# Optimization experiments

Measured on AMD Instinct MI355X. Metric: run time of the kernel, lower is better.

The kernel has to match this reference:

```python
import jax, jax.numpy as jnp
import numpy as np

B, S, DIM, HEADS, EXPERTS = 2, 2048, 1024, 16, 8
DFF = 4 * DIM
EPS = 1e-5


def setup_inputs() -> dict:
    key = jax.random.key(0)
    ks = jax.random.split(key, 16)
    w = lambda k, shp: jax.random.normal(k, shp, dtype=jnp.float32) * 0.02
    return {
        "x": jax.random.normal(ks[0], (B, S, DIM), dtype=jnp.float32),
        "ln1_g": jnp.ones((DIM,), jnp.float32), "ln1_b": jnp.zeros((DIM,), jnp.float32),
        "ln2_g": jnp.ones((DIM,), jnp.float32), "ln2_b": jnp.zeros((DIM,), jnp.float32),
        "wq": w(ks[1], (DIM, DIM)), "bq": jnp.zeros((DIM,), jnp.float32),
        "wk": w(ks[2], (DIM, DIM)), "bk": jnp.zeros((DIM,), jnp.float32),
        "wv": w(ks[3], (DIM, DIM)), "bv": jnp.zeros((DIM,), jnp.float32),
        "wo": w(ks[4], (DIM, DIM)), "bo": jnp.zeros((DIM,), jnp.float32),
        "w1": w(ks[5], (EXPERTS, DIM, DFF)), "b1": jnp.zeros((EXPERTS, DFF), jnp.float32),
        "w2": w(ks[6], (EXPERTS, DFF, DIM)), "b2": jnp.zeros((EXPERTS, DIM), jnp.float32),
        "token_split": np.full(EXPERTS, S // EXPERTS, dtype=np.int64),  # static split sizes
        "heads": HEADS,
    }


def _layernorm(h, g, b):
    m = h.mean(-1, keepdims=True)
    v = ((h - m) ** 2).mean(-1, keepdims=True)
    return (h - m) * jax.lax.rsqrt(v + EPS) * g + b


def reference(x, ln1_g, ln1_b, ln2_g, ln2_b, wq, bq, wk, bk, wv, bv, wo, bo,
              w1, b1, w2, b2, token_split, heads):
    Bx, Sx, D = x.shape
    Dh = D // heads
    # --- attention on norm1(x) ---
    h = _layernorm(x, ln1_g, ln1_b)
    q = (h @ wq + bq).reshape(Bx, Sx, heads, Dh)
    k = (h @ wk + bk).reshape(Bx, Sx, heads, Dh)
    v = (h @ wv + bv).reshape(Bx, Sx, heads, Dh)
    scores = jnp.einsum('bqhd,bkhd->bhqk', q, k) * (Dh ** -0.5)
    attn = jax.nn.softmax(scores, axis=-1)
    o = jnp.einsum('bhqk,bkhd->bqhd', attn, v).reshape(Bx, Sx, D)
    x = x + (o @ wo + bo)
    # --- token-chunked per-expert MLP ---
    residual = x
    h = _layernorm(x, ln2_g, ln2_b)
    split_pts = np.cumsum(np.asarray(token_split))[:-1]  # static boundaries
    chunks = jnp.split(h, split_pts, axis=1)
    outs = [jax.nn.silu(c @ w1[e] + b1[e]) @ w2[e] + b2[e]
            for e, c in enumerate(chunks)]
    return jnp.concatenate(outs, axis=1) + residual
```

## Files before the change

### kernel.cpp

```cpp
#include <hip/hip_runtime.h>


typedef unsigned int  u32;
typedef unsigned short u16;
typedef short v8s __attribute__((ext_vector_type(8)));
typedef float v4f __attribute__((ext_vector_type(4)));

#define SEQ  2048
#define DIM_ 1024
#define EPS_ 1e-5f

__device__ __forceinline__ u16 f2bf(float f) {
    __bf16 h = (__bf16)f;
    return __builtin_bit_cast(u16, h);
}

__device__ __forceinline__ void gload16(const void* g, void* l) {
    __builtin_amdgcn_global_load_lds((const __attribute__((address_space(1))) u32*)g,
                                     (__attribute__((address_space(3))) u32*)l, 16, 0, 0);
}

__global__ __launch_bounds__(256) void ln_kernel(const float* __restrict__ x,
                                                 const float* __restrict__ g,
                                                 const float* __restrict__ b,
                                                 u16* __restrict__ out) {
    int row = blockIdx.x;
    int t = threadIdx.x;
    const float4* xr = (const float4*)(x + (size_t)row * DIM_);
    float4 v = xr[t];
    float s  = v.x + v.y + v.z + v.w;
    float ss = v.x*v.x + v.y*v.y + v.z*v.z + v.w*v.w;
    #pragma unroll
    for (int off = 32; off > 0; off >>= 1) {
        s  += __shfl_down(s, off);
        ss += __shfl_down(ss, off);
    }
    __shared__ float red[8];
    if ((t & 63) == 0) { red[t >> 6] = s; red[4 + (t >> 6)] = ss; }
    __syncthreads();
    s  = red[0] + red[1] + red[2] + red[3];
    ss = red[4] + red[5] + red[6] + red[7];
    float mean = s * (1.0f / DIM_);
    float var  = ss * (1.0f / DIM_) - mean * mean;
    float rstd = rsqrtf(var + EPS_);
    float4 gv = ((const float4*)g)[t];
    float4 bv = ((const float4*)b)[t];
    ushort4 ov;
    ov.x = f2bf((v.x - mean) * rstd * gv.x + bv.x);
    ov.y = f2bf((v.y - mean) * rstd * gv.y + bv.y);
    ov.z = f2bf((v.z - mean) * rstd * gv.z + bv.z);
    ov.w = f2bf((v.w - mean) * rstd * gv.w + bv.w);
    *(ushort4*)(out + (size_t)row * DIM_ + t * 4) = ov;
}

template<int BN, int ACT, bool GROUPED, int WMODE>
__global__ __launch_bounds__(256) void gemm_bf16(
    const u16* __restrict__ A,
    const float* __restrict__ W0, const float* __restrict__ Wk, const float* __restrict__ Wv,
    const float* __restrict__ b0, const float* __restrict__ bk2, const float* __restrict__ bv2,
    const float* __restrict__ resid, float* __restrict__ Cf,
    u16* __restrict__ Cb, u16* __restrict__ Ckb, u16* __restrict__ vtb,
    int Nw, int K)
{
    constexpr int BM = 128;
    constexpr int MI = 4;
    constexpr int NI = BN / 32;
    constexpr int SL = BN / 32;
    __shared__ __attribute__((aligned(16))) char AsB[BM * 128];
    __shared__ __attribute__((aligned(16))) char BsB[BN * 128];

    int tid = threadIdx.x;
    int lane = tid & 63, w = tid >> 6;
    int wr = w >> 1, wc = w & 1;
    int g = lane >> 4, lq = lane & 15;

    long row0; const float* W = W0; const float* bias = b0;
    if (GROUPED) {
        int seg = blockIdx.y >> 1, mh = blockIdx.y & 1;
        int bb = seg >> 3, e = seg & 7;
        row0 = (long)bb * SEQ + e * 256 + mh * BM;
        W += (size_t)e * K * Nw; bias += (size_t)e * Nw;
    } else row0 = (long)blockIdx.y * BM;

    int col0 = blockIdx.x * BN;
    int colL = col0;
    if (WMODE == 2) {
        int sel = col0 >> 10; colL = col0 & 1023;
        if (sel == 1)      { W = Wk; bias = bk2; }
        else if (sel == 2) { W = Wv; bias = bv2; }
    }

    const u16* Arow = A + row0 * K;

    v4f acc[MI][NI];
    #pragma unroll
    for (int mi = 0; mi < MI; mi++)
        #pragma unroll
        for (int ni = 0; ni < NI; ni++) acc[mi][ni] = (v4f){0.f, 0.f, 0.f, 0.f};

    int nB = tid & (BN - 1);
    int sgB = tid / BN;

    for (int kt = 0; kt < K; kt += 64) {
        #pragma unroll
        for (int i = 0; i < 4; i++) {
            int row  = (i * 4 + w) * 8 + (lane >> 3);
            int scol = ((lane & 7) ^ (row & 7)) << 3;
            gload16(Arow + (size_t)row * K + kt + scol, AsB + (i * 4 + w) * 1024);
        }
        #pragma unroll
        for (int i = 0; i < SL; i++) {
            int s = sgB * SL + i;
            float fv[8];
            #pragma unroll
            for (int j = 0; j < 8; j++)
                fv[j] = W[(size_t)(kt + s * 8 + j) * Nw + colL + nB];
            union { v8s v; u16 u[8]; } pk;
            #pragma unroll
            for (int j = 0; j < 8; j++) pk.u[j] = f2bf(fv[j]);
            *(v8s*)(BsB + nB * 128 + ((s ^ (nB & 7)) << 4)) = pk.v;
        }
        __syncthreads();
        #pragma unroll
        for (int kk = 0; kk < 64; kk += 32) {
            v8s af[MI], bfv[NI];
            int slot = (kk >> 3) + g;
            #pragma unroll
            for (int mi = 0; mi < MI; mi++) {
                int row = wr * 64 + mi * 16 + lq;
                af[mi] = *(const v8s*)(AsB + row * 128 + ((slot ^ (row & 7)) << 4));
            }
            #pragma unroll
            for (int ni = 0; ni < NI; ni++) {
                int rn = wc * (BN / 2) + ni * 16 + lq;
                bfv[ni] = *(const v8s*)(BsB + rn * 128 + ((slot ^ (rn & 7)) << 4));
            }
            #pragma unroll
            for (int mi = 0; mi < MI; mi++)
                #pragma unroll
                for (int ni = 0; ni < NI; ni++)
                    acc[mi][ni] = __builtin_amdgcn_mfma_f32_16x16x32_bf16(
                        af[mi], bfv[ni], acc[mi][ni], 0, 0, 0);
        }
        __syncthreads();
    }

    #pragma unroll
    for (int mi = 0; mi < MI; mi++) {
        int grow = wr * 64 + mi * 16 + g * 4;
        #pragma unroll
        for (int ni = 0; ni < NI; ni++) {
            int cL = colL + wc * (BN / 2) + ni * 16 + lq;
            float bb_ = bias[cL];
            v4f a = acc[mi][ni];
            if (WMODE == 0) {
                #pragma unroll
                for (int r = 0; r < 4; r++) {
                    float val = a[r] + bb_;
                    if (ACT == 1) val = val / (1.0f + __expf(-val));
                    size_t idx = (size_t)(row0 + grow + r) * Nw + cL;
                    val += resid[idx];
                    Cf[idx] = val;
                }
            } else if (WMODE == 1) {
                #pragma unroll
                for (int r = 0; r < 4; r++) {
                    float val = a[r] + bb_;
                    if (ACT == 1) val = val / (1.0f + __expf(-val));
                    Cb[(size_t)(row0 + grow + r) * Nw + cL] = f2bf(val);
                }
            } else {
                int sel = col0 >> 10;
                if (sel < 2) {
                    u16* dst = (sel == 0) ? Cb : Ckb;
                    #pragma unroll
                    for (int r = 0; r < 4; r++)
                        dst[(size_t)(row0 + grow + r) * 1024 + cL] = f2bf(a[r] + bb_);
                } else {
                    long token0 = row0 + grow;
                    int bb2 = (int)(token0 >> 11);
                    int ss  = (int)(token0 & 2047);
                    int hh = cL >> 6, dd = cL & 63;
                    ushort4 pv_;
                    pv_.x = f2bf(a[0] + bb_); pv_.y = f2bf(a[1] + bb_);
                    pv_.z = f2bf(a[2] + bb_); pv_.w = f2bf(a[3] + bb_);
                    *(ushort4*)(vtb + ((size_t)(bb2 * 16 + hh) * 64 + dd) * 2048 + ss) = pv_;
                }
            }
        }
    }
}

__global__ __launch_bounds__(256) void attn_kernel(const u16* __restrict__ qb,
                                                   const u16* __restrict__ kb,
                                                   const u16* __restrict__ vtb,
                                                   u16* __restrict__ ob) {
    __shared__ __attribute__((aligned(16))) char Kl[8192];
    __shared__ __attribute__((aligned(16))) char Vl[8192];
    __shared__ __attribute__((aligned(16))) char Pl[4][4608];

    int tid = threadIdx.x;
    int lane = tid & 63, w = tid >> 6;
    int g = lane >> 4, lq = lane & 15;
    int h = blockIdx.y, bz = blockIdx.z;
    int q0 = blockIdx.x * 128 + w * 32;
    const size_t hb = (size_t)h * 64;

    v8s qfr[2][2];
    #pragma unroll
    for (int qi = 0; qi < 2; qi++)
        #pragma unroll
        for (int kkh = 0; kkh < 2; kkh++)
            qfr[qi][kkh] = *(const v8s*)(qb + ((size_t)(bz * SEQ + q0 + qi * 16 + lq)) * DIM_
                                         + hb + kkh * 32 + g * 8);

    v4f oacc[2][4];
    #pragma unroll
    for (int qi = 0; qi < 2; qi++)
        #pragma unroll
        for (int df = 0; df < 4; df++) oacc[qi][df] = (v4f){0.f, 0.f, 0.f, 0.f};
    float m_prev[2] = {-1e30f, -1e30f}, l_acc[2] = {0.f, 0.f};

    for (int kv = 0; kv < SEQ; kv += 64) {
        __syncthreads();
        #pragma unroll
        for (int i = 0; i < 2; i++) {
            int beta = (i * 4 + w) * 1024 + lane * 16;
            int row  = beta >> 7;
            int sc   = ((lane & 7) ^ (row & 7)) << 3;
            gload16(kb + ((size_t)(bz * SEQ + kv + row)) * DIM_ + hb + sc,
                    Kl + (i * 4 + w) * 1024);
            gload16(vtb + ((size_t)((bz * 16 + h) * 64 + row)) * 2048 + kv + sc,
                    Vl + (i * 4 + w) * 1024);
        }
        __syncthreads();

        v4f sa[4][2];
        #pragma unroll
        for (int cf = 0; cf < 4; cf++)
            #pragma unroll
            for (int qi = 0; qi < 2; qi++) sa[cf][qi] = (v4f){0.f, 0.f, 0.f, 0.f};
        #pragma unroll
        for (int kkh = 0; kkh < 2; kkh++) {
            v8s kf[4];
            int slot = kkh * 4 + g;
            #pragma unroll
            for (int cf = 0; cf < 4; cf++) {
                int row = cf * 16 + lq;
                kf[cf] = *(const v8s*)(Kl + row * 128 + ((slot ^ (row & 7)) << 4));
            }
            #pragma unroll
            for (int cf = 0; cf < 4; cf++)
                #pragma unroll
                for (int qi = 0; qi < 2; qi++)
                    sa[cf][qi] = __builtin_amdgcn_mfma_f32_16x16x32_bf16(
                        kf[cf], qfr[qi][kkh], sa[cf][qi], 0, 0, 0);
        }

        #pragma unroll
        for (int qi = 0; qi < 2; qi++) {
            float mx = -1e30f;
            #pragma unroll
            for (int cf = 0; cf < 4; cf++)
                #pragma unroll
                for (int r = 0; r < 4; r++) mx = fmaxf(mx, sa[cf][qi][r]);
            mx = fmaxf(mx, __shfl_xor(mx, 16));
            mx = fmaxf(mx, __shfl_xor(mx, 32));
            float rm = mx * 0.125f;
            if (__any(rm - m_prev[qi] > 8.0f)) {
                float mnew = fmaxf(m_prev[qi], rm);
                float corr = __expf(m_prev[qi] - mnew);
                m_prev[qi] = mnew;
                l_acc[qi] *= corr;
                #pragma unroll
                for (int r = 0; r < 4; r++) {
                    float cr = __shfl(corr, (lane & 48) | (g * 4 + r));
                    #pragma unroll
                    for (int df = 0; df < 4; df++) oacc[qi][df][r] *= cr;
                }
            }
            float rs = 0.f;
            float ps[4][4];
            #pragma unroll
            for (int cf = 0; cf < 4; cf++)
                #pragma unroll
                for (int r = 0; r < 4; r++) {
                    float p = __expf(sa[cf][qi][r] * 0.125f - m_prev[qi]);
                    ps[cf][r] = p; rs += p;
                }
            rs += __shfl_xor(rs, 16);
            rs += __shfl_xor(rs, 32);
            l_acc[qi] += rs;
            #pragma unroll
            for (int cf = 0; cf < 4; cf++) {
                ushort4 pw;
                pw.x = f2bf(ps[cf][0]); pw.y = f2bf(ps[cf][1]);
                pw.z = f2bf(ps[cf][2]); pw.w = f2bf(ps[cf][3]);
                *(ushort4*)(Pl[w] + (qi * 16 + lq) * 144 + (cf * 16 + g * 4) * 2) = pw;
            }
        }
        asm volatile("s_waitcnt lgkmcnt(0)" ::: "memory");
        __builtin_amdgcn_sched_barrier(0);

        #pragma unroll
        for (int kkh = 0; kkh < 2; kkh++) {
            v8s pa[2], vf[4];
            int slot = kkh * 4 + g;
            #pragma unroll
            for (int qi = 0; qi < 2; qi++)
                pa[qi] = *(const v8s*)(Pl[w] + (qi * 16 + lq) * 144 + kkh * 64 + g * 16);
            #pragma unroll
            for (int df = 0; df < 4; df++) {
                int row = df * 16 + lq;
                vf[df] = *(const v8s*)(Vl + row * 128 + ((slot ^ (row & 7)) << 4));
            }
            #pragma unroll
            for (int qi = 0; qi < 2; qi++)
                #pragma unroll
                for (int df = 0; df < 4; df++)
                    oacc[qi][df] = __builtin_amdgcn_mfma_f32_16x16x32_bf16(
                        pa[qi], vf[df], oacc[qi][df], 0, 0, 0);
        }
    }

    #pragma unroll
    for (int qi = 0; qi < 2; qi++) {
        float inv = 1.0f / l_acc[qi];
        #pragma unroll
        for (int r = 0; r < 4; r++) {
            float ivr = __shfl(inv, (lane & 48) | (g * 4 + r));
            size_t rowi = (size_t)(bz * SEQ + q0 + qi * 16 + g * 4 + r) * DIM_ + hb;
            #pragma unroll
            for (int df = 0; df < 4; df++)
                ob[rowi + df * 16 + lq] = f2bf(oacc[qi][df][r] * ivr);
        }
    }
}

extern "C" void kernel_launch(void* const* d_in, const int* in_sizes, int n_in,
                              void* d_out, int out_size, void* d_ws, size_t ws_size,
                              hipStream_t stream) {
    const float* x     = (const float*)d_in[0];
    const float* ln1_g = (const float*)d_in[1];
    const float* ln1_b = (const float*)d_in[2];
    const float* ln2_g = (const float*)d_in[3];
    const float* ln2_b = (const float*)d_in[4];
    const float* wq = (const float*)d_in[5];  const float* bq = (const float*)d_in[6];
    const float* wk = (const float*)d_in[7];  const float* bk = (const float*)d_in[8];
    const float* wv = (const float*)d_in[9];  const float* bv = (const float*)d_in[10];
    const float* wo = (const float*)d_in[11]; const float* bo = (const float*)d_in[12];
    const float* w1 = (const float*)d_in[13]; const float* b1 = (const float*)d_in[14];
    const float* w2 = (const float*)d_in[15]; const float* b2 = (const float*)d_in[16];

    char* wsb = (char*)d_ws;
    const size_t MB = 1024 * 1024;
    u16*   h1  = (u16*)(wsb + 0 * MB);
    u16*   qbf = (u16*)(wsb + 8 * MB);
    u16*   kbf = (u16*)(wsb + 16 * MB);
    u16*   vt  = (u16*)(wsb + 24 * MB);
    float* x2  = (float*)(wsb + 32 * MB);
    u16*   mid = (u16*)(wsb + 48 * MB);
    u16*   ob  = h1;
    u16*   h2  = qbf;
    float* outp = (float*)d_out;

    ln_kernel<<<4096, 256, 0, stream>>>(x, ln1_g, ln1_b, h1);

    gemm_bf16<128, 0, false, 2><<<dim3(24, 32), 256, 0, stream>>>(
        h1, wq, wk, wv, bq, bk, bv, nullptr, nullptr, qbf, kbf, vt, 1024, 1024);

    attn_kernel<<<dim3(16, 16, 2), 256, 0, stream>>>(qbf, kbf, vt, ob);

    gemm_bf16<64, 0, false, 0><<<dim3(16, 32), 256, 0, stream>>>(
        ob, wo, nullptr, nullptr, bo, nullptr, nullptr, x, x2,
        nullptr, nullptr, nullptr, 1024, 1024);

    ln_kernel<<<4096, 256, 0, stream>>>(x2, ln2_g, ln2_b, h2);

    gemm_bf16<128, 1, true, 1><<<dim3(32, 32), 256, 0, stream>>>(
        h2, w1, nullptr, nullptr, b1, nullptr, nullptr, nullptr, nullptr,
        mid, nullptr, nullptr, 4096, 1024);

    gemm_bf16<64, 0, true, 0><<<dim3(16, 32), 256, 0, stream>>>(
        mid, w2, nullptr, nullptr, b2, nullptr, nullptr, x2, outp,
        nullptr, nullptr, nullptr, 1024, 4096);
}
```

Before: 589.5 us.

## Pre-convert weights to transposed bf16 and stream B tiles via async LDS loads

Adds a transpose-and-convert kernel that turns the fp32 attention and expert weights into bf16 [N][K] copies in workspace at the start of each call. The GEMM kernel then fetches B tiles with the same swizzled global_load_lds path used for A, replacing per-thread strided fp32 loads and in-kernel bf16 conversion. This is meant to remove the redundant fp32 weight reads and conversion work repeated by every row block. The trade-off is an extra pass that reads all weights and writes bf16 copies, including roughly 128 MB of expert weights, plus workspace buffers that reuse overlapping regions.

```diff
diff --git a/kernel.cpp b/kernel.cpp
--- a/kernel.cpp
+++ b/kernel.cpp
@@ -18,6 +18,42 @@
 __device__ __forceinline__ void gload16(const void* g, void* l) {
     __builtin_amdgcn_global_load_lds((const __attribute__((address_space(1))) u32*)g,
                                      (__attribute__((address_space(3))) u32*)l, 16, 0, 0);
+}
+
+template<bool SEP>
+__global__ __launch_bounds__(256) void conv_t(const float* __restrict__ s0,
+                                              const float* __restrict__ s1,
+                                              const float* __restrict__ s2,
+                                              const float* __restrict__ s3,
+                                              u16* __restrict__ dst, int K, int N) {
+    __shared__ __attribute__((aligned(16))) u16 Ts[64][72];
+    int tid = threadIdx.x;
+    int z = blockIdx.z;
+    const float* src = SEP ? (z == 0 ? s0 : z == 1 ? s1 : z == 2 ? s2 : s3)
+                           : s0 + (size_t)z * K * N;
+    u16* d = dst + (size_t)z * K * N;
+    int k0 = blockIdx.y * 64, n0 = blockIdx.x * 64;
+    int tk = tid >> 4, tn = tid & 15;
+
+    u16 t[4][4];
+    #pragma unroll
+    for (int r = 0; r < 4; r++) {
+        float4 L = *(const float4*)&src[(size_t)(k0 + tk * 4 + r) * N + n0 + tn * 4];
+        t[r][0] = f2bf(L.x); t[r][1] = f2bf(L.y); t[r][2] = f2bf(L.z); t[r][3] = f2bf(L.w);
+    }
+    #pragma unroll
+    for (int c = 0; c < 4; c++) {
+        ushort4 q4 = { t[0][c], t[1][c], t[2][c], t[3][c] };
+        *(ushort4*)&Ts[tn * 4 + c][tk * 4] = q4;
+    }
+    __syncthreads();
+    #pragma unroll
+    for (int i = 0; i < 2; i++) {
+        int id = tid + i * 256;
+        int row = id >> 3, ch = id & 7;
+        v8s val = *(const v8s*)&Ts[row][ch * 8];
+        *(v8s*)&d[(size_t)(n0 + row) * K + k0 + ch * 8] = val;
+    }
 }
 
 __global__ __launch_bounds__(256) void ln_kernel(const float* __restrict__ x,
@@ -55,8 +91,7 @@
 
 template<int BN, int ACT, bool GROUPED, int WMODE>
 __global__ __launch_bounds__(256) void gemm_bf16(
-    const u16* __restrict__ A,
-    const float* __restrict__ W0, const float* __restrict__ Wk, const float* __restrict__ Wv,
+    const u16* __restrict__ A, const u16* __restrict__ WT,
     const float* __restrict__ b0, const float* __restrict__ bk2, const float* __restrict__ bv2,
     const float* __restrict__ resid, float* __restrict__ Cf,
     u16* __restrict__ Cb, u16* __restrict__ Ckb, u16* __restrict__ vtb,
@@ -65,7 +100,6 @@
     constexpr int BM = 128;
     constexpr int MI = 4;
     constexpr int NI = BN / 32;
-    constexpr int SL = BN / 32;
     __shared__ __attribute__((aligned(16))) char AsB[BM * 128];
     __shared__ __attribute__((aligned(16))) char BsB[BN * 128];
 
@@ -74,23 +108,25 @@
     int wr = w >> 1, wc = w & 1;
     int g = lane >> 4, lq = lane & 15;
 
-    long row0; const float* W = W0; const float* bias = b0;
+    long row0; int e = 0;
+    const float* bias = b0;
     if (GROUPED) {
         int seg = blockIdx.y >> 1, mh = blockIdx.y & 1;
-        int bb = seg >> 3, e = seg & 7;
+        int bb = seg >> 3; e = seg & 7;
         row0 = (long)bb * SEQ + e * 256 + mh * BM;
-        W += (size_t)e * K * Nw; bias += (size_t)e * Nw;
+        bias += (size_t)e * Nw;
     } else row0 = (long)blockIdx.y * BM;
 
     int col0 = blockIdx.x * BN;
     int colL = col0;
     if (WMODE == 2) {
         int sel = col0 >> 10; colL = col0 & 1023;
-        if (sel == 1)      { W = Wk; bias = bk2; }
-        else if (sel == 2) { W = Wv; bias = bv2; }
-    }
-
-    const u16* Arow = A + row0 * K;
+        if (sel == 1)      bias = bk2;
+        else if (sel == 2) bias = bv2;
+    }
+
+    const u16* Arow = A + (size_t)row0 * K;
+    const u16* Brow = WT + (GROUPED ? ((size_t)e * Nw + col0) : (size_t)col0) * K;
 
     v4f acc[MI][NI];
     #pragma unroll
@@ -98,27 +134,20 @@
         #pragma unroll
         for (int ni = 0; ni < NI; ni++) acc[mi][ni] = (v4f){0.f, 0.f, 0.f, 0.f};
 
-    int nB = tid & (BN - 1);
-    int sgB = tid / BN;
-
     for (int kt = 0; kt < K; kt += 64) {
         #pragma unroll
         for (int i = 0; i < 4; i++) {
-            int row  = (i * 4 + w) * 8 + (lane >> 3);
-            int scol = ((lane & 7) ^ (row & 7)) << 3;
-            gload16(Arow + (size_t)row * K + kt + scol, AsB + (i * 4 + w) * 1024);
-        }
-        #pragma unroll
-        for (int i = 0; i < SL; i++) {
-            int s = sgB * SL + i;
-            float fv[8];
-            #pragma unroll
-            for (int j = 0; j < 8; j++)
-                fv[j] = W[(size_t)(kt + s * 8 + j) * Nw + colL + nB];
-            union { v8s v; u16 u[8]; } pk;
-            #pragma unroll
-            for (int j = 0; j < 8; j++) pk.u[j] = f2bf(fv[j]);
-            *(v8s*)(BsB + nB * 128 + ((s ^ (nB & 7)) << 4)) = pk.v;
+            int R0 = (i * 4 + w) * 8;
+            int row = R0 + (lane >> 3);
+            gload16(Arow + (size_t)row * K + kt + (((lane & 7) ^ (row & 7)) << 3),
+                    AsB + R0 * 128);
+        }
+        #pragma unroll
+        for (int i = 0; i < NI; i++) {
+            int R0 = (i * 4 + w) * 8;
+            int row = R0 + (lane >> 3);
+            gload16(Brow + (size_t)row * K + kt + (((lane & 7) ^ (row & 7)) << 3),
+                    BsB + R0 * 128);
         }
         __syncthreads();
         #pragma unroll
@@ -354,34 +383,42 @@
 
     char* wsb = (char*)d_ws;
     const size_t MB = 1024 * 1024;
-    u16*   h1  = (u16*)(wsb + 0 * MB);
-    u16*   qbf = (u16*)(wsb + 8 * MB);
-    u16*   kbf = (u16*)(wsb + 16 * MB);
-    u16*   vt  = (u16*)(wsb + 24 * MB);
-    float* x2  = (float*)(wsb + 32 * MB);
-    u16*   mid = (u16*)(wsb + 48 * MB);
-    u16*   ob  = h1;
-    u16*   h2  = qbf;
+    u16*   h1   = (u16*)(wsb + 0 * MB);
+    u16*   qbf  = (u16*)(wsb + 8 * MB);
+    u16*   kbf  = (u16*)(wsb + 16 * MB);
+    u16*   vt   = (u16*)(wsb + 24 * MB);
+    float* x2   = (float*)(wsb + 32 * MB);
+    u16*   wqkvoT = (u16*)(wsb + 48 * MB);
+    u16*   mid  = (u16*)(wsb + 48 * MB);
+    u16*   w1T  = (u16*)(wsb + 80 * MB);
+    u16*   w2T  = (u16*)(wsb + 80 * MB);
+    u16*   ob   = h1;
+    u16*   h2   = qbf;
     float* outp = (float*)d_out;
 
+    conv_t<true ><<<dim3(16, 16, 4), 256, 0, stream>>>(wq, wk, wv, wo, wqkvoT, 1024, 1024);
+    conv_t<false><<<dim3(64, 16, 8), 256, 0, stream>>>(w1, nullptr, nullptr, nullptr, w1T, 1024, 4096);
+
     ln_kernel<<<4096, 256, 0, stream>>>(x, ln1_g, ln1_b, h1);
 
     gemm_bf16<128, 0, false, 2><<<dim3(24, 32), 256, 0, stream>>>(
-        h1, wq, wk, wv, bq, bk, bv, nullptr, nullptr, qbf, kbf, vt, 1024, 1024);
+        h1, wqkvoT, bq, bk, bv, nullptr, nullptr, qbf, kbf, vt, 1024, 1024);
 
     attn_kernel<<<dim3(16, 16, 2), 256, 0, stream>>>(qbf, kbf, vt, ob);
 
     gemm_bf16<64, 0, false, 0><<<dim3(16, 32), 256, 0, stream>>>(
-        ob, wo, nullptr, nullptr, bo, nullptr, nullptr, x, x2,
+        ob, wqkvoT + (size_t)3 * 1024 * 1024, bo, nullptr, nullptr, x, x2,
         nullptr, nullptr, nullptr, 1024, 1024);
 
     ln_kernel<<<4096, 256, 0, stream>>>(x2, ln2_g, ln2_b, h2);
 
     gemm_bf16<128, 1, true, 1><<<dim3(32, 32), 256, 0, stream>>>(
-        h2, w1, nullptr, nullptr, b1, nullptr, nullptr, nullptr, nullptr,
+        h2, w1T, b1, nullptr, nullptr, nullptr, nullptr,
         mid, nullptr, nullptr, 4096, 1024);
 
+    conv_t<false><<<dim3(16, 64, 8), 256, 0, stream>>>(w2, nullptr, nullptr, nullptr, w2T, 4096, 1024);
+
     gemm_bf16<64, 0, true, 0><<<dim3(16, 32), 256, 0, stream>>>(
-        mid, w2, nullptr, nullptr, b2, nullptr, nullptr, x2, outp,
+        mid, w2T, b2, nullptr, nullptr, x2, outp,
         nullptr, nullptr, nullptr, 1024, 4096);
 }
```

After: 596.9 us. No clear change (+1.3%).
